# Kernel tuning notes

Hardware: AMD Instinct MI355X
Metric: run time of the kernel (lower is better)

## Reference

```python
import jax, jax.numpy as jnp
import numpy as np

M = 6           # Anderson memory slots (init default)
THRESHOLD = 30  # max forward iterations (forward default)
LAM = 1e-4      # Tikhonov regularization lambda
BETA = 1.0      # learn_beta=False -> beta=1.0 every step


def setup_inputs() -> dict:
    key = jax.random.key(0)
    k1, k2, k3 = jax.random.split(key, 3)
    bsz, d = 2048, 2048
    x0 = jax.random.normal(k1, (bsz, d), jnp.float32)
    # f(x) = tanh(x @ W + b): a contraction-ish layer standing in for the user-supplied f
    W = jax.random.normal(k2, (d, d), jnp.float32) * 0.02
    b = jax.random.normal(k3, (d,), jnp.float32)
    return {"x0": x0, "W": W, "b": b}


def reference(x0, W, b):
    def f(x):
        return jnp.tanh(x @ W + b)

    bsz, d = x0.shape
    m, threshold, lam, beta = M, THRESHOLD, LAM, BETA

    # Eval-mode circular buffers of size m (self.training == False branch)
    X = jnp.zeros((bsz, m, d), x0.dtype).at[:, 0].set(x0)
    F = jnp.zeros((bsz, m, d), x0.dtype).at[:, 0].set(f(x0))
    # torch: F = F.detach(); X = X.detach() (initial entries carry no grad)
    X = jax.lax.stop_gradient(X)
    F = jax.lax.stop_gradient(F)

    # x0 is random nonzero -> (x0 == 0).all() is False -> k_start = 1
    abs_trace, rel_trace = [], []
    eye_m = jnp.eye(m, dtype=x0.dtype)
    up = 0
    for k in range(1, threshold):  # fixed-count unrolled loop; n is static per step
        n = min(k, m)
        up = k % m
        G = F[:, :n] - X[:, :n]                                  # [bsz, n, d]
        GGt = jnp.einsum('bnd,bmd->bnm', G, G) + lam * eye_m[:n, :n]
        # Bordered system H: [[0, 1^T], [1, GG^T + lam I]], y = e_0
        H = (jnp.zeros((bsz, n + 1, n + 1), x0.dtype)
             .at[:, 0, 1:].set(1.0)
             .at[:, 1:, 0].set(1.0)
             .at[:, 1:, 1:].set(GGt))
        y = jnp.zeros((bsz, n + 1, 1), x0.dtype).at[:, 0, 0].set(1.0)
        alpha = jnp.linalg.solve(H, y)[:, 1:, 0]                 # [bsz, n]
        xnew = (beta * jnp.einsum('bn,bnd->bd', alpha, F[:, :n])
                + (1.0 - beta) * jnp.einsum('bn,bnd->bd', alpha, X[:, :n]))
        fnew = f(xnew)
        X = X.at[:, up].set(xnew)
        F = F.at[:, up].set(fnew)
        gx = fnew - xnew
        abs_diff = jnp.linalg.norm(gx)
        rel_diff = abs_diff / (1e-5 + jnp.linalg.norm(fnew))
        abs_trace.append(abs_diff)
        rel_trace.append(rel_diff)

    result = X[:, up]  # 'result' in the torch dict
    rel = jnp.stack(rel_trace).reshape(1, -1)
    absd = jnp.stack(abs_trace).reshape(1, -1)
    return result, X, rel, absd
```

## Files before the change

kernel.cpp:

```cpp
#include <hip/hip_runtime.h>
#include <math.h>

#define BSZ 2048
#define DIM 2048
#define MS 6
#define NIT 29
#define LAMREG 1e-4f
#define XROWS (MS*DIM)

typedef __bf16 bf16x8 __attribute__((ext_vector_type(8)));
typedef __bf16 bf16x4 __attribute__((ext_vector_type(4)));
typedef float  f32x4  __attribute__((ext_vector_type(4)));

__device__ __forceinline__ void async16(const void* g, void* l) {
    __builtin_amdgcn_global_load_lds((const __attribute__((address_space(1))) void*)g,
                                     (__attribute__((address_space(3))) void*)l, 16, 0, 0);
}

__device__ __forceinline__ int swz(int r, int q) {
    return r * 32 + ((q ^ ((r >> 1) & 3)) << 3);
}

__global__ __launch_bounds__(256) void init_kernel(const float* __restrict__ x0,
                                                   float* __restrict__ Xout,
                                                   __bf16* __restrict__ Ahi,
                                                   __bf16* __restrict__ Alo,
                                                   float* __restrict__ norms) {
    int idx = blockIdx.x * 256 + threadIdx.x;
    if (idx < 2 * NIT) norms[idx] = 0.0f;
    for (int i = idx; i < BSZ * DIM; i += gridDim.x * 256) {
        int b = i >> 11;
        int j = i & (DIM - 1);
        float v = x0[i];
        Xout[(size_t)b * XROWS + j] = v;
        __bf16 h = (__bf16)v;
        Ahi[i] = h;
        Alo[i] = (__bf16)(v - (float)h);
    }
}

__global__ __launch_bounds__(256) void wt_split_kernel(const float* __restrict__ W,
                                                       __bf16* __restrict__ WThi,
                                                       __bf16* __restrict__ WTlo) {
    __shared__ float tile[32][33];
    const int tx = threadIdx.x & 31;
    const int ty = threadIdx.x >> 5;
    const int n0 = blockIdx.x * 32;
    const int k0 = blockIdx.y * 32;
#pragma unroll
    for (int i = 0; i < 32; i += 8)
        tile[ty + i][tx] = W[(size_t)(k0 + ty + i) * DIM + n0 + tx];
    __syncthreads();
#pragma unroll
    for (int i = 0; i < 32; i += 8) {
        float v = tile[tx][ty + i];
        __bf16 h = (__bf16)v;
        size_t o = (size_t)(n0 + ty + i) * DIM + k0 + tx;
        WThi[o] = h;
        WTlo[o] = (__bf16)(v - (float)h);
    }
}

__global__ __launch_bounds__(256, 2) void gemm_mfma_kernel(
    const __bf16* __restrict__ Ahi, const __bf16* __restrict__ Alo,
    const __bf16* __restrict__ WThi, const __bf16* __restrict__ WTlo,
    const float* __restrict__ bias,
    const float* __restrict__ Xbase, float* __restrict__ Fbase,
    float* __restrict__ Gbase, int up,
    float* __restrict__ normAcc, int doNorm)
{
    __shared__ __align__(16) __bf16 Ah[2][128 * 32];
    __shared__ __align__(16) __bf16 Al[2][128 * 32];
    __shared__ __align__(16) __bf16 Bh[2][64 * 32];
    __shared__ __align__(16) __bf16 Bl[2][64 * 32];
    __shared__ float rs[8];

    const int id = blockIdx.x;
    const int xcd = id & 7;
    const int slot = id >> 3;
    const int by = ((xcd & 1) << 3) | (slot & 7);
    const int bx = ((xcd >> 1) << 3) | (slot >> 3);
    const int m0 = by * 128;
    const int n0 = bx * 64;

    const int tid = threadIdx.x;
    const int l = tid & 63;
    const int w = tid >> 6;
    const int wm = (w & 1) * 64;
    const int wn = (w >> 1) * 32;
    const int rl = l & 15;
    const int quad = l >> 4;

    const int srow = w * 16 + (l >> 2);
    const int gchunk = (l & 3) ^ ((l >> 3) & 3);
    const int scol = gchunk << 3;
    const size_t aoff = (size_t)(m0 + srow) * DIM + scol;
    const size_t boff = (size_t)(n0 + srow) * DIM + scol;
    const int lo = w * 512;

    f32x4 acc[4][2];
#pragma unroll
    for (int t = 0; t < 4; t++)
#pragma unroll
        for (int u = 0; u < 2; u++) acc[t][u] = (f32x4){0.f, 0.f, 0.f, 0.f};

    auto stage = [&](int kb, int s) {
        async16(Ahi + aoff + kb, &Ah[s][lo]);
        async16(Ahi + aoff + (size_t)64 * DIM + kb, &Ah[s][lo + 2048]);
        async16(Alo + aoff + kb, &Al[s][lo]);
        async16(Alo + aoff + (size_t)64 * DIM + kb, &Al[s][lo + 2048]);
        async16(WThi + boff + kb, &Bh[s][lo]);
        async16(WTlo + boff + kb, &Bl[s][lo]);
    };
    auto compute = [&](int s) {
        bf16x8 ah[4], al[4];
#pragma unroll
        for (int t = 0; t < 4; t++) {
            const int r = wm + t * 16 + rl;
            ah[t] = *(const bf16x8*)&Ah[s][swz(r, quad)];
            al[t] = *(const bf16x8*)&Al[s][swz(r, quad)];
        }
#pragma unroll
        for (int u = 0; u < 2; u++) {
            const int c = wn + u * 16 + rl;
            bf16x8 bh = *(const bf16x8*)&Bh[s][swz(c, quad)];
            bf16x8 bl = *(const bf16x8*)&Bl[s][swz(c, quad)];
#pragma unroll
            for (int t = 0; t < 4; t++) {
                acc[t][u] = __builtin_amdgcn_mfma_f32_16x16x32_bf16(ah[t], bh, acc[t][u], 0, 0, 0);
                acc[t][u] = __builtin_amdgcn_mfma_f32_16x16x32_bf16(al[t], bh, acc[t][u], 0, 0, 0);
                acc[t][u] = __builtin_amdgcn_mfma_f32_16x16x32_bf16(ah[t], bl, acc[t][u], 0, 0, 0);
            }
        }
    };

    stage(0, 0);
    for (int k0 = 0; k0 < DIM; k0 += 64) {
        __syncthreads();
        stage(k0 + 32, 1);
        compute(0);
        __syncthreads();
        if (k0 + 64 < DIM) stage(k0 + 64, 0);
        compute(1);
    }

    int cols[2]; float bv[2];
#pragma unroll
    for (int u = 0; u < 2; u++) {
        cols[u] = n0 + wn + u * 16 + rl;
        bv[u] = bias[cols[u]];
    }
    float s1 = 0.0f, s2 = 0.0f;
#pragma unroll
    for (int t = 0; t < 4; t++) {
#pragma unroll
        for (int r = 0; r < 4; r++) {
            const int row = m0 + wm + t * 16 + quad * 4 + r;
            const size_t base = (size_t)row * XROWS + (size_t)up * DIM;
#pragma unroll
            for (int u = 0; u < 2; u++) {
                float v = tanhf(acc[t][u][r] + bv[u]);
                float xv = Xbase[base + cols[u]];
                float g = v - xv;
                Fbase[base + cols[u]] = v;
                if (Gbase) Gbase[base + cols[u]] = g;
                if (doNorm) { s1 = fmaf(g, g, s1); s2 = fmaf(v, v, s2); }
            }
        }
    }
    if (doNorm) {
#pragma unroll
        for (int off = 32; off > 0; off >>= 1) {
            s1 += __shfl_down(s1, off);
            s2 += __shfl_down(s2, off);
        }
        if (l == 0) { rs[w * 2] = s1; rs[w * 2 + 1] = s2; }
        __syncthreads();
        if (tid == 0) {
            atomicAdd(&normAcc[0], rs[0] + rs[2] + rs[4] + rs[6]);
            atomicAdd(&normAcc[1], rs[1] + rs[3] + rs[5] + rs[7]);
        }
    }
}

__global__ __launch_bounds__(256) void dots_solve_kernel(
    const float* __restrict__ F, const float* __restrict__ X,
    const float* __restrict__ G, float* __restrict__ GGt,
    float* __restrict__ alpha, int up, int nact)
{
    const int b = blockIdx.x;
    const int tid = threadIdx.x;
    const size_t rb = (size_t)b * XROWS;
    float acc[MS];
#pragma unroll
    for (int p = 0; p < MS; p++) acc[p] = 0.0f;

    if (G) {
        const f32x4* Gb = (const f32x4*)(G + rb);
        for (int pos = tid; pos < DIM / 4; pos += 256) {
            f32x4 gu = Gb[up * (DIM / 4) + pos];
#pragma unroll
            for (int j = 0; j < MS; j++) {
                if (j < nact) {
                    f32x4 gj = (j == up) ? gu : Gb[j * (DIM / 4) + pos];
                    acc[j] = fmaf(gu.x, gj.x, acc[j]);
                    acc[j] = fmaf(gu.y, gj.y, acc[j]);
                    acc[j] = fmaf(gu.z, gj.z, acc[j]);
                    acc[j] = fmaf(gu.w, gj.w, acc[j]);
                }
            }
        }
    } else {
        const f32x4* Fb = (const f32x4*)(F + rb);
        const f32x4* Xb = (const f32x4*)(X + rb);
        for (int pos = tid; pos < DIM / 4; pos += 256) {
            f32x4 fu = Fb[up * (DIM / 4) + pos];
            f32x4 xu = Xb[up * (DIM / 4) + pos];
            f32x4 gu = fu - xu;
#pragma unroll
            for (int j = 0; j < MS; j++) {
                if (j < nact) {
                    f32x4 gj;
                    if (j == up) gj = gu;
                    else {
                        f32x4 fj = Fb[j * (DIM / 4) + pos];
                        f32x4 xj = Xb[j * (DIM / 4) + pos];
                        gj = fj - xj;
                    }
                    acc[j] = fmaf(gu.x, gj.x, acc[j]);
                    acc[j] = fmaf(gu.y, gj.y, acc[j]);
                    acc[j] = fmaf(gu.z, gj.z, acc[j]);
                    acc[j] = fmaf(gu.w, gj.w, acc[j]);
                }
            }
        }
    }

#pragma unroll
    for (int p = 0; p < MS; p++) {
        float v = acc[p];
#pragma unroll
        for (int off = 32; off > 0; off >>= 1) v += __shfl_down(v, off);
        acc[p] = v;
    }
    __shared__ float red[4][MS];
    __shared__ float Hs[7][8];
    __shared__ float sols[7];
    const int lane = tid & 63, wave = tid >> 6;
    if (lane == 0) {
#pragma unroll
        for (int p = 0; p < MS; p++) red[wave][p] = acc[p];
    }
    __syncthreads();
    if (tid == 0) {
        float d[MS];
#pragma unroll
        for (int j = 0; j < MS; j++)
            d[j] = red[0][j] + red[1][j] + red[2][j] + red[3][j];
        float* gg = GGt + (size_t)b * 36;
        for (int j = 0; j < nact; j++) {
            gg[up * 6 + j] = d[j];
            gg[j * 6 + up] = d[j];
        }
        const int np = nact + 1;
        for (int i = 0; i < np; i++) {
            for (int j = 0; j < np; j++) {
                float v;
                if (i == 0 && j == 0) v = 0.0f;
                else if (i == 0 || j == 0) v = 1.0f;
                else {
                    v = gg[(i - 1) * 6 + (j - 1)];
                    if (i == j) v += LAMREG;
                }
                Hs[i][j] = v;
            }
            Hs[i][7] = (i == 0) ? 1.0f : 0.0f;
        }
        for (int c = 0; c < np; c++) {
            int piv = c;
            float mx = fabsf(Hs[c][c]);
            for (int r = c + 1; r < np; r++) {
                float a = fabsf(Hs[r][c]);
                if (a > mx) { mx = a; piv = r; }
            }
            if (piv != c) {
                for (int cc = c; cc <= 7; cc++) {
                    float t = Hs[c][cc]; Hs[c][cc] = Hs[piv][cc]; Hs[piv][cc] = t;
                }
            }
            float inv = 1.0f / Hs[c][c];
            for (int r = c + 1; r < np; r++) {
                float f = Hs[r][c] * inv;
                for (int cc = c; cc <= 7; cc++) Hs[r][cc] -= f * Hs[c][cc];
            }
        }
        for (int c = np - 1; c >= 0; c--) {
            float s = Hs[c][7];
            for (int cc = c + 1; cc < np; cc++) s -= Hs[c][cc] * sols[cc];
            sols[c] = s / Hs[c][c];
        }
        for (int i = 0; i < nact; i++) alpha[(size_t)b * MS + i] = sols[i + 1];
    }
}

__global__ __launch_bounds__(256) void xnew_kernel(
    const float* __restrict__ F, const float* __restrict__ alpha,
    float* __restrict__ Xout, __bf16* __restrict__ Ahi, __bf16* __restrict__ Alo,
    float* __restrict__ resultOrNull, int n, int up)
{
    const int idx = blockIdx.x * 256 + threadIdx.x;
    const int b = idx >> 9;
    const int j4 = idx & 511;
    const float* al = alpha + (size_t)b * MS;
    const f32x4* fb = (const f32x4*)(F + (size_t)b * XROWS);
    f32x4 s = (f32x4){0.f, 0.f, 0.f, 0.f};
    for (int i = 0; i < n; i++) {
        f32x4 fv = fb[i * (DIM / 4) + j4];
        float a = al[i];
        s.x = fmaf(a, fv.x, s.x);
        s.y = fmaf(a, fv.y, s.y);
        s.z = fmaf(a, fv.z, s.z);
        s.w = fmaf(a, fv.w, s.w);
    }
    *(f32x4*)(Xout + (size_t)b * XROWS + (size_t)up * DIM + (size_t)j4 * 4) = s;
    if (resultOrNull) ((f32x4*)resultOrNull)[idx] = s;
    bf16x4 hh, ll;
#pragma unroll
    for (int c = 0; c < 4; c++) {
        float v = s[c];
        __bf16 h = (__bf16)v;
        hh[c] = h;
        ll[c] = (__bf16)(v - (float)h);
    }
    *(bf16x4*)&Ahi[(size_t)idx * 4] = hh;
    *(bf16x4*)&Alo[(size_t)idx * 4] = ll;
}

__global__ void finalize_kernel(const float* __restrict__ norms,
                                float* __restrict__ rel, float* __restrict__ absd)
{
    int t = threadIdx.x;
    if (t < NIT) {
        float a = sqrtf(norms[2 * t]);
        float fn = sqrtf(norms[2 * t + 1]);
        absd[t] = a;
        rel[t] = a / (1e-5f + fn);
    }
}

extern "C" void kernel_launch(void* const* d_in, const int* in_sizes, int n_in,
                              void* d_out, int out_size, void* d_ws, size_t ws_size,
                              hipStream_t stream) {
    const float* x0   = (const float*)d_in[0];
    const float* W    = (const float*)d_in[1];
    const float* bias = (const float*)d_in[2];

    float* out    = (float*)d_out;
    float* result = out;
    float* Xout   = out + (size_t)BSZ * DIM;
    float* rel    = Xout + (size_t)BSZ * MS * DIM;
    float* absd   = rel + NIT;

    char* ws = (char*)d_ws;
    float* F     = (float*)ws;
    float* alpha = F + (size_t)BSZ * MS * DIM;
    float* norms = alpha + (size_t)BSZ * MS;
    float* GGt   = norms + 64;
    char* p = (char*)(GGt + (size_t)BSZ * 36);
    size_t off = ((size_t)(p - ws) + 255) & ~(size_t)255;
    __bf16* Ahi  = (__bf16*)(ws + off);  off += (size_t)BSZ * DIM * 2;
    __bf16* Alo  = (__bf16*)(ws + off);  off += (size_t)BSZ * DIM * 2;
    __bf16* WThi = (__bf16*)(ws + off);  off += (size_t)DIM * DIM * 2;
    __bf16* WTlo = (__bf16*)(ws + off);  off += (size_t)DIM * DIM * 2;
    float* G = nullptr;
    if (ws_size >= off + (size_t)BSZ * MS * DIM * 4 + 256) {
        off = (off + 255) & ~(size_t)255;
        G = (float*)(ws + off);
    }

    wt_split_kernel<<<dim3(64, 64), 256, 0, stream>>>(W, WThi, WTlo);
    init_kernel<<<2048, 256, 0, stream>>>(x0, Xout, Ahi, Alo, norms);
    gemm_mfma_kernel<<<512, 256, 0, stream>>>(Ahi, Alo, WThi, WTlo, bias,
                                              Xout, F, G, 0, nullptr, 0);
    dots_solve_kernel<<<BSZ, 256, 0, stream>>>(F, Xout, G, GGt, alpha, 0, 1);
    for (int k = 1; k <= NIT; k++) {
        int n = (k < MS) ? k : MS;
        int up = k % MS;
        int nact = (k + 1 < MS) ? (k + 1) : MS;
        xnew_kernel<<<BSZ * DIM / 1024, 256, 0, stream>>>(F, alpha, Xout, Ahi, Alo,
                                                          (k == NIT) ? result : nullptr,
                                                          n, up);
        gemm_mfma_kernel<<<512, 256, 0, stream>>>(Ahi, Alo, WThi, WTlo, bias,
                                                  Xout, F, G, up,
                                                  norms + 2 * (k - 1), 1);
        if (k < NIT)
            dots_solve_kernel<<<BSZ, 256, 0, stream>>>(F, Xout, G, GGt, alpha, up, nact);
    }
    finalize_kernel<<<1, 64, 0, stream>>>(norms, rel, absd);
}
```

Before: 4.469 ms.

## Split-K GEMM with 128x128 tiles and fuse epilogue, dots, solve, xnew per row

The GEMM now uses 128x128 tiles with a 2-way split over K and writes raw fp32 partials to a scratch buffer. A new per-row mega kernel sums the partials, adds the bias and applies tanh, writes F and G, computes the Gram dot products and norms, solves the small bordered system, and forms the next x with its bf16 hi/lo split. This replaces three kernels per iteration with two. It removes the separate xnew pass and repeated F reads, and spreads the norm atomics over 8 slots. In exchange it adds a round trip of two full fp32 partial matrices through memory, and the serial solve now sits inside a kernel that also streams row data.

```diff
diff --git a/kernel.cpp b/kernel.cpp
--- a/kernel.cpp
+++ b/kernel.cpp
@@ -7,6 +7,7 @@
 #define NIT 29
 #define LAMREG 1e-4f
 #define XROWS (MS*DIM)
+#define N2 ((size_t)BSZ*DIM)
 
 typedef __bf16 bf16x8 __attribute__((ext_vector_type(8)));
 typedef __bf16 bf16x4 __attribute__((ext_vector_type(4)));
@@ -27,7 +28,7 @@
                                                    __bf16* __restrict__ Alo,
                                                    float* __restrict__ norms) {
     int idx = blockIdx.x * 256 + threadIdx.x;
-    if (idx < 2 * NIT) norms[idx] = 0.0f;
+    if (idx < 16 * NIT) norms[idx] = 0.0f;
     for (int i = idx; i < BSZ * DIM; i += gridDim.x * 256) {
         int b = i >> 11;
         int j = i & (DIM - 1);
@@ -64,45 +65,44 @@
 __global__ __launch_bounds__(256, 2) void gemm_mfma_kernel(
     const __bf16* __restrict__ Ahi, const __bf16* __restrict__ Alo,
     const __bf16* __restrict__ WThi, const __bf16* __restrict__ WTlo,
-    const float* __restrict__ bias,
-    const float* __restrict__ Xbase, float* __restrict__ Fbase,
-    float* __restrict__ Gbase, int up,
-    float* __restrict__ normAcc, int doNorm)
+    float* __restrict__ P)
 {
     __shared__ __align__(16) __bf16 Ah[2][128 * 32];
     __shared__ __align__(16) __bf16 Al[2][128 * 32];
-    __shared__ __align__(16) __bf16 Bh[2][64 * 32];
-    __shared__ __align__(16) __bf16 Bl[2][64 * 32];
-    __shared__ float rs[8];
+    __shared__ __align__(16) __bf16 Bh[2][128 * 32];
+    __shared__ __align__(16) __bf16 Bl[2][128 * 32];
 
     const int id = blockIdx.x;
     const int xcd = id & 7;
-    const int slot = id >> 3;
-    const int by = ((xcd & 1) << 3) | (slot & 7);
-    const int bx = ((xcd >> 1) << 3) | (slot >> 3);
+    const int rest = id >> 3;
+    const int ks = rest >> 5;
+    const int slot = rest & 31;
+    const int by = ((xcd & 3) << 2) | (slot & 3);
+    const int bx = ((xcd >> 2) << 3) | (slot >> 2);
     const int m0 = by * 128;
-    const int n0 = bx * 64;
+    const int n0 = bx * 128;
+    const int kbase = ks << 10;
 
     const int tid = threadIdx.x;
     const int l = tid & 63;
     const int w = tid >> 6;
     const int wm = (w & 1) * 64;
-    const int wn = (w >> 1) * 32;
+    const int wn = (w >> 1) * 64;
     const int rl = l & 15;
     const int quad = l >> 4;
 
     const int srow = w * 16 + (l >> 2);
     const int gchunk = (l & 3) ^ ((l >> 3) & 3);
     const int scol = gchunk << 3;
-    const size_t aoff = (size_t)(m0 + srow) * DIM + scol;
-    const size_t boff = (size_t)(n0 + srow) * DIM + scol;
+    const size_t aoff = (size_t)(m0 + srow) * DIM + kbase + scol;
+    const size_t boff = (size_t)(n0 + srow) * DIM + kbase + scol;
     const int lo = w * 512;
 
-    f32x4 acc[4][2];
+    f32x4 acc[4][4];
 #pragma unroll
     for (int t = 0; t < 4; t++)
 #pragma unroll
-        for (int u = 0; u < 2; u++) acc[t][u] = (f32x4){0.f, 0.f, 0.f, 0.f};
+        for (int u = 0; u < 4; u++) acc[t][u] = (f32x4){0.f, 0.f, 0.f, 0.f};
 
     auto stage = [&](int kb, int s) {
         async16(Ahi + aoff + kb, &Ah[s][lo]);
@@ -110,7 +110,9 @@
         async16(Alo + aoff + kb, &Al[s][lo]);
         async16(Alo + aoff + (size_t)64 * DIM + kb, &Al[s][lo + 2048]);
         async16(WThi + boff + kb, &Bh[s][lo]);
+        async16(WThi + boff + (size_t)64 * DIM + kb, &Bh[s][lo + 2048]);
         async16(WTlo + boff + kb, &Bl[s][lo]);
+        async16(WTlo + boff + (size_t)64 * DIM + kb, &Bl[s][lo + 2048]);
     };
     auto compute = [&](int s) {
         bf16x8 ah[4], al[4];
@@ -121,7 +123,7 @@
             al[t] = *(const bf16x8*)&Al[s][swz(r, quad)];
         }
 #pragma unroll
-        for (int u = 0; u < 2; u++) {
+        for (int u = 0; u < 4; u++) {
             const int c = wn + u * 16 + rl;
             bf16x8 bh = *(const bf16x8*)&Bh[s][swz(c, quad)];
             bf16x8 bl = *(const bf16x8*)&Bl[s][swz(c, quad)];
@@ -135,205 +137,217 @@
     };
 
     stage(0, 0);
-    for (int k0 = 0; k0 < DIM; k0 += 64) {
+    for (int k0 = 0; k0 < 1024; k0 += 64) {
         __syncthreads();
         stage(k0 + 32, 1);
         compute(0);
         __syncthreads();
-        if (k0 + 64 < DIM) stage(k0 + 64, 0);
+        if (k0 + 64 < 1024) stage(k0 + 64, 0);
         compute(1);
     }
 
-    int cols[2]; float bv[2];
-#pragma unroll
-    for (int u = 0; u < 2; u++) {
-        cols[u] = n0 + wn + u * 16 + rl;
-        bv[u] = bias[cols[u]];
-    }
-    float s1 = 0.0f, s2 = 0.0f;
+    float* Pk = P + (size_t)ks * N2;
 #pragma unroll
     for (int t = 0; t < 4; t++) {
 #pragma unroll
         for (int r = 0; r < 4; r++) {
             const int row = m0 + wm + t * 16 + quad * 4 + r;
-            const size_t base = (size_t)row * XROWS + (size_t)up * DIM;
-#pragma unroll
-            for (int u = 0; u < 2; u++) {
-                float v = tanhf(acc[t][u][r] + bv[u]);
-                float xv = Xbase[base + cols[u]];
-                float g = v - xv;
-                Fbase[base + cols[u]] = v;
-                if (Gbase) Gbase[base + cols[u]] = g;
-                if (doNorm) { s1 = fmaf(g, g, s1); s2 = fmaf(v, v, s2); }
-            }
-        }
-    }
-    if (doNorm) {
-#pragma unroll
-        for (int off = 32; off > 0; off >>= 1) {
-            s1 += __shfl_down(s1, off);
-            s2 += __shfl_down(s2, off);
-        }
-        if (l == 0) { rs[w * 2] = s1; rs[w * 2 + 1] = s2; }
-        __syncthreads();
-        if (tid == 0) {
-            atomicAdd(&normAcc[0], rs[0] + rs[2] + rs[4] + rs[6]);
-            atomicAdd(&normAcc[1], rs[1] + rs[3] + rs[5] + rs[7]);
-        }
-    }
-}
-
-__global__ __launch_bounds__(256) void dots_solve_kernel(
-    const float* __restrict__ F, const float* __restrict__ X,
-    const float* __restrict__ G, float* __restrict__ GGt,
-    float* __restrict__ alpha, int up, int nact)
+            float* pr = Pk + (size_t)row * DIM + n0 + wn;
+#pragma unroll
+            for (int u = 0; u < 4; u++) pr[u * 16 + rl] = acc[t][u][r];
+        }
+    }
+}
+
+__global__ __launch_bounds__(256) void mega_kernel(
+    const float* __restrict__ P, const float* __restrict__ bias,
+    float* __restrict__ Fb, float* __restrict__ Xb, float* __restrict__ Gb,
+    float* __restrict__ GGt,
+    __bf16* __restrict__ Ahi, __bf16* __restrict__ Alo,
+    float* __restrict__ resultOrNull, float* __restrict__ normAcc,
+    int up, int nact, int nxt)
 {
     const int b = blockIdx.x;
     const int tid = threadIdx.x;
     const size_t rb = (size_t)b * XROWS;
-    float acc[MS];
-#pragma unroll
-    for (int p = 0; p < MS; p++) acc[p] = 0.0f;
-
-    if (G) {
-        const f32x4* Gb = (const f32x4*)(G + rb);
-        for (int pos = tid; pos < DIM / 4; pos += 256) {
-            f32x4 gu = Gb[up * (DIM / 4) + pos];
-#pragma unroll
-            for (int j = 0; j < MS; j++) {
-                if (j < nact) {
-                    f32x4 gj = (j == up) ? gu : Gb[j * (DIM / 4) + pos];
-                    acc[j] = fmaf(gu.x, gj.x, acc[j]);
-                    acc[j] = fmaf(gu.y, gj.y, acc[j]);
-                    acc[j] = fmaf(gu.z, gj.z, acc[j]);
-                    acc[j] = fmaf(gu.w, gj.w, acc[j]);
-                }
-            }
-        }
-    } else {
-        const f32x4* Fb = (const f32x4*)(F + rb);
-        const f32x4* Xb = (const f32x4*)(X + rb);
-        for (int pos = tid; pos < DIM / 4; pos += 256) {
-            f32x4 fu = Fb[up * (DIM / 4) + pos];
-            f32x4 xu = Xb[up * (DIM / 4) + pos];
-            f32x4 gu = fu - xu;
-#pragma unroll
-            for (int j = 0; j < MS; j++) {
-                if (j < nact) {
-                    f32x4 gj;
-                    if (j == up) gj = gu;
-                    else {
-                        f32x4 fj = Fb[j * (DIM / 4) + pos];
-                        f32x4 xj = Xb[j * (DIM / 4) + pos];
-                        gj = fj - xj;
+    const size_t prow = (size_t)b * DIM;
+
+    const f32x4* P0 = (const f32x4*)(P + prow);
+    const f32x4* P1 = (const f32x4*)(P + N2 + prow);
+    const f32x4* Bi = (const f32x4*)bias;
+    const f32x4* Xu = (const f32x4*)(Xb + rb + (size_t)up * DIM);
+    f32x4* Fu = (f32x4*)(Fb + rb + (size_t)up * DIM);
+    f32x4* Gu = Gb ? (f32x4*)(Gb + rb + (size_t)up * DIM) : nullptr;
+
+    f32x4 fv[2], gv[2];
+    float s1 = 0.f, s2 = 0.f;
+#pragma unroll
+    for (int i = 0; i < 2; i++) {
+        const int p4 = tid + 256 * i;
+        f32x4 z = P0[p4] + P1[p4] + Bi[p4];
+        f32x4 t;
+        t.x = tanhf(z.x); t.y = tanhf(z.y); t.z = tanhf(z.z); t.w = tanhf(z.w);
+        f32x4 xv = Xu[p4];
+        f32x4 g = t - xv;
+        fv[i] = t; gv[i] = g;
+        Fu[p4] = t;
+        if (Gu) Gu[p4] = g;
+        s1 += g.x * g.x + g.y * g.y + g.z * g.z + g.w * g.w;
+        s2 += t.x * t.x + t.y * t.y + t.z * t.z + t.w * t.w;
+    }
+
+    float acc[8];
+#pragma unroll
+    for (int p = 0; p < MS; p++) acc[p] = 0.f;
+    acc[6] = s1; acc[7] = s2;
+
+    if (nact > 0) {
+#pragma unroll
+        for (int j = 0; j < MS; j++) {
+            if (j < nact) {
+                if (j == up) { acc[j] = s1; continue; }
+                float a = 0.f;
+                if (Gb) {
+                    const f32x4* Gj = (const f32x4*)(Gb + rb + (size_t)j * DIM);
+#pragma unroll
+                    for (int i = 0; i < 2; i++) {
+                        const int p4 = tid + 256 * i;
+                        f32x4 gj = Gj[p4];
+                        a += gv[i].x * gj.x + gv[i].y * gj.y + gv[i].z * gj.z + gv[i].w * gj.w;
                     }
-                    acc[j] = fmaf(gu.x, gj.x, acc[j]);
-                    acc[j] = fmaf(gu.y, gj.y, acc[j]);
-                    acc[j] = fmaf(gu.z, gj.z, acc[j]);
-                    acc[j] = fmaf(gu.w, gj.w, acc[j]);
-                }
-            }
-        }
-    }
-
-#pragma unroll
-    for (int p = 0; p < MS; p++) {
+                } else {
+                    const f32x4* Fj = (const f32x4*)(Fb + rb + (size_t)j * DIM);
+                    const f32x4* Xj = (const f32x4*)(Xb + rb + (size_t)j * DIM);
+#pragma unroll
+                    for (int i = 0; i < 2; i++) {
+                        const int p4 = tid + 256 * i;
+                        f32x4 gj = Fj[p4] - Xj[p4];
+                        a += gv[i].x * gj.x + gv[i].y * gj.y + gv[i].z * gj.z + gv[i].w * gj.w;
+                    }
+                }
+                acc[j] = a;
+            }
+        }
+    }
+
+#pragma unroll
+    for (int p = 0; p < 8; p++) {
         float v = acc[p];
 #pragma unroll
         for (int off = 32; off > 0; off >>= 1) v += __shfl_down(v, off);
         acc[p] = v;
     }
-    __shared__ float red[4][MS];
+    __shared__ float red[4][8];
     __shared__ float Hs[7][8];
-    __shared__ float sols[7];
+    __shared__ float alf[7];
     const int lane = tid & 63, wave = tid >> 6;
     if (lane == 0) {
 #pragma unroll
-        for (int p = 0; p < MS; p++) red[wave][p] = acc[p];
+        for (int p = 0; p < 8; p++) red[wave][p] = acc[p];
     }
     __syncthreads();
+
     if (tid == 0) {
-        float d[MS];
-#pragma unroll
-        for (int j = 0; j < MS; j++)
-            d[j] = red[0][j] + red[1][j] + red[2][j] + red[3][j];
-        float* gg = GGt + (size_t)b * 36;
-        for (int j = 0; j < nact; j++) {
-            gg[up * 6 + j] = d[j];
-            gg[j * 6 + up] = d[j];
-        }
-        const int np = nact + 1;
-        for (int i = 0; i < np; i++) {
-            for (int j = 0; j < np; j++) {
-                float v;
-                if (i == 0 && j == 0) v = 0.0f;
-                else if (i == 0 || j == 0) v = 1.0f;
-                else {
-                    v = gg[(i - 1) * 6 + (j - 1)];
-                    if (i == j) v += LAMREG;
-                }
-                Hs[i][j] = v;
-            }
-            Hs[i][7] = (i == 0) ? 1.0f : 0.0f;
-        }
-        for (int c = 0; c < np; c++) {
-            int piv = c;
-            float mx = fabsf(Hs[c][c]);
-            for (int r = c + 1; r < np; r++) {
-                float a = fabsf(Hs[r][c]);
-                if (a > mx) { mx = a; piv = r; }
-            }
-            if (piv != c) {
-                for (int cc = c; cc <= 7; cc++) {
-                    float t = Hs[c][cc]; Hs[c][cc] = Hs[piv][cc]; Hs[piv][cc] = t;
-                }
-            }
-            float inv = 1.0f / Hs[c][c];
-            for (int r = c + 1; r < np; r++) {
-                float f = Hs[r][c] * inv;
-                for (int cc = c; cc <= 7; cc++) Hs[r][cc] -= f * Hs[c][cc];
-            }
-        }
-        for (int c = np - 1; c >= 0; c--) {
-            float s = Hs[c][7];
-            for (int cc = c + 1; cc < np; cc++) s -= Hs[c][cc] * sols[cc];
-            sols[c] = s / Hs[c][c];
-        }
-        for (int i = 0; i < nact; i++) alpha[(size_t)b * MS + i] = sols[i + 1];
-    }
-}
-
-__global__ __launch_bounds__(256) void xnew_kernel(
-    const float* __restrict__ F, const float* __restrict__ alpha,
-    float* __restrict__ Xout, __bf16* __restrict__ Ahi, __bf16* __restrict__ Alo,
-    float* __restrict__ resultOrNull, int n, int up)
-{
-    const int idx = blockIdx.x * 256 + threadIdx.x;
-    const int b = idx >> 9;
-    const int j4 = idx & 511;
-    const float* al = alpha + (size_t)b * MS;
-    const f32x4* fb = (const f32x4*)(F + (size_t)b * XROWS);
-    f32x4 s = (f32x4){0.f, 0.f, 0.f, 0.f};
-    for (int i = 0; i < n; i++) {
-        f32x4 fv = fb[i * (DIM / 4) + j4];
-        float a = al[i];
-        s.x = fmaf(a, fv.x, s.x);
-        s.y = fmaf(a, fv.y, s.y);
-        s.z = fmaf(a, fv.z, s.z);
-        s.w = fmaf(a, fv.w, s.w);
-    }
-    *(f32x4*)(Xout + (size_t)b * XROWS + (size_t)up * DIM + (size_t)j4 * 4) = s;
-    if (resultOrNull) ((f32x4*)resultOrNull)[idx] = s;
-    bf16x4 hh, ll;
-#pragma unroll
-    for (int c = 0; c < 4; c++) {
-        float v = s[c];
-        __bf16 h = (__bf16)v;
-        hh[c] = h;
-        ll[c] = (__bf16)(v - (float)h);
-    }
-    *(bf16x4*)&Ahi[(size_t)idx * 4] = hh;
-    *(bf16x4*)&Alo[(size_t)idx * 4] = ll;
+        float d[8];
+#pragma unroll
+        for (int p = 0; p < 8; p++)
+            d[p] = red[0][p] + red[1][p] + red[2][p] + red[3][p];
+        if (normAcc) {
+            atomicAdd(&normAcc[b & 7], d[6]);
+            atomicAdd(&normAcc[8 + (b & 7)], d[7]);
+        }
+        if (nact > 0) {
+            float* gg = GGt + (size_t)b * 36;
+            for (int j = 0; j < nact; j++) {
+                gg[up * 6 + j] = d[j];
+                gg[j * 6 + up] = d[j];
+            }
+            const int np = nact + 1;
+            for (int i = 0; i < np; i++) {
+                for (int j = 0; j < np; j++) {
+                    float v;
+                    if (i == 0 && j == 0) v = 0.0f;
+                    else if (i == 0 || j == 0) v = 1.0f;
+                    else {
+                        v = gg[(i - 1) * 6 + (j - 1)];
+                        if (i == j) v += LAMREG;
+                    }
+                    Hs[i][j] = v;
+                }
+                Hs[i][7] = (i == 0) ? 1.0f : 0.0f;
+            }
+            for (int c = 0; c < np; c++) {
+                int piv = c;
+                float mx = fabsf(Hs[c][c]);
+                for (int r = c + 1; r < np; r++) {
+                    float a = fabsf(Hs[r][c]);
+                    if (a > mx) { mx = a; piv = r; }
+                }
+                if (piv != c) {
+                    for (int cc = c; cc <= 7; cc++) {
+                        float t = Hs[c][cc]; Hs[c][cc] = Hs[piv][cc]; Hs[piv][cc] = t;
+                    }
+                }
+                float inv = 1.0f / Hs[c][c];
+                for (int r = c + 1; r < np; r++) {
+                    float f = Hs[r][c] * inv;
+                    for (int cc = c; cc <= 7; cc++) Hs[r][cc] -= f * Hs[c][cc];
+                }
+            }
+            float sol[7];
+            for (int c = np - 1; c >= 0; c--) {
+                float s = Hs[c][7];
+                for (int cc = c + 1; cc < np; cc++) s -= Hs[c][cc] * sol[cc];
+                sol[c] = s / Hs[c][c];
+            }
+            for (int i = 0; i < nact; i++) alf[i] = sol[i + 1];
+        }
+    }
+    __syncthreads();
+
+    if (nxt >= 0) {
+        f32x4 s[2] = {(f32x4){0.f,0.f,0.f,0.f}, (f32x4){0.f,0.f,0.f,0.f}};
+        for (int i2 = 0; i2 < nact; i2++) {
+            const float a = alf[i2];
+            if (i2 == up) {
+#pragma unroll
+                for (int i = 0; i < 2; i++) {
+                    s[i].x = fmaf(a, fv[i].x, s[i].x);
+                    s[i].y = fmaf(a, fv[i].y, s[i].y);
+                    s[i].z = fmaf(a, fv[i].z, s[i].z);
+                    s[i].w = fmaf(a, fv[i].w, s[i].w);
+                }
+            } else {
+                const f32x4* Fi = (const f32x4*)(Fb + rb + (size_t)i2 * DIM);
+#pragma unroll
+                for (int i = 0; i < 2; i++) {
+                    const int p4 = tid + 256 * i;
+                    f32x4 fj = Fi[p4];
+                    s[i].x = fmaf(a, fj.x, s[i].x);
+                    s[i].y = fmaf(a, fj.y, s[i].y);
+                    s[i].z = fmaf(a, fj.z, s[i].z);
+                    s[i].w = fmaf(a, fj.w, s[i].w);
+                }
+            }
+        }
+        f32x4* Xn = (f32x4*)(Xb + rb + (size_t)nxt * DIM);
+#pragma unroll
+        for (int i = 0; i < 2; i++) {
+            const int p4 = tid + 256 * i;
+            Xn[p4] = s[i];
+            if (resultOrNull) ((f32x4*)(resultOrNull + prow))[p4] = s[i];
+            bf16x4 hh, ll;
+#pragma unroll
+            for (int c = 0; c < 4; c++) {
+                float v = s[i][c];
+                __bf16 h = (__bf16)v;
+                hh[c] = h;
+                ll[c] = (__bf16)(v - (float)h);
+            }
+            *(bf16x4*)&Ahi[prow + (size_t)p4 * 4] = hh;
+            *(bf16x4*)&Alo[prow + (size_t)p4 * 4] = ll;
+        }
+    }
 }
 
 __global__ void finalize_kernel(const float* __restrict__ norms,
@@ -341,10 +355,14 @@
 {
     int t = threadIdx.x;
     if (t < NIT) {
-        float a = sqrtf(norms[2 * t]);
-        float fn = sqrtf(norms[2 * t + 1]);
+        float a2 = 0.f, f2 = 0.f;
+        for (int i = 0; i < 8; i++) {
+            a2 += norms[t * 16 + i];
+            f2 += norms[t * 16 + 8 + i];
+        }
+        float a = sqrtf(a2);
         absd[t] = a;
-        rel[t] = a / (1e-5f + fn);
+        rel[t] = a / (1e-5f + sqrtf(f2));
     }
 }
 
@@ -363,10 +381,10 @@
 
     char* ws = (char*)d_ws;
     float* F     = (float*)ws;
-    float* alpha = F + (size_t)BSZ * MS * DIM;
-    float* norms = alpha + (size_t)BSZ * MS;
-    float* GGt   = norms + 64;
-    char* p = (char*)(GGt + (size_t)BSZ * 36);
+    float* norms = F + (size_t)BSZ * MS * DIM;
+    float* GGt   = norms + 512;
+    float* P     = GGt + (size_t)BSZ * 36;
+    char* p = (char*)(P + 2 * N2);
     size_t off = ((size_t)(p - ws) + 255) & ~(size_t)255;
     __bf16* Ahi  = (__bf16*)(ws + off);  off += (size_t)BSZ * DIM * 2;
     __bf16* Alo  = (__bf16*)(ws + off);  off += (size_t)BSZ * DIM * 2;
@@ -380,21 +398,16 @@
 
     wt_split_kernel<<<dim3(64, 64), 256, 0, stream>>>(W, WThi, WTlo);
     init_kernel<<<2048, 256, 0, stream>>>(x0, Xout, Ahi, Alo, norms);
-    gemm_mfma_kernel<<<512, 256, 0, stream>>>(Ahi, Alo, WThi, WTlo, bias,
-                                              Xout, F, G, 0, nullptr, 0);
-    dots_solve_kernel<<<BSZ, 256, 0, stream>>>(F, Xout, G, GGt, alpha, 0, 1);
-    for (int k = 1; k <= NIT; k++) {
-        int n = (k < MS) ? k : MS;
-        int up = k % MS;
-        int nact = (k + 1 < MS) ? (k + 1) : MS;
-        xnew_kernel<<<BSZ * DIM / 1024, 256, 0, stream>>>(F, alpha, Xout, Ahi, Alo,
-                                                          (k == NIT) ? result : nullptr,
-                                                          n, up);
-        gemm_mfma_kernel<<<512, 256, 0, stream>>>(Ahi, Alo, WThi, WTlo, bias,
-                                                  Xout, F, G, up,
-                                                  norms + 2 * (k - 1), 1);
-        if (k < NIT)
-            dots_solve_kernel<<<BSZ, 256, 0, stream>>>(F, Xout, G, GGt, alpha, up, nact);
+
+    for (int j = 0; j <= NIT; j++) {
+        gemm_mfma_kernel<<<512, 256, 0, stream>>>(Ahi, Alo, WThi, WTlo, P);
+        int up   = j % MS;
+        int nact = (j < NIT) ? ((j + 1 < MS) ? (j + 1) : MS) : 0;
+        int nxt  = (j < NIT) ? ((j + 1) % MS) : -1;
+        mega_kernel<<<BSZ, 256, 0, stream>>>(P, bias, F, Xout, G, GGt, Ahi, Alo,
+                                             (j == NIT - 1) ? result : nullptr,
+                                             (j >= 1) ? (norms + 16 * (j - 1)) : nullptr,
+                                             up, nact, nxt);
     }
     finalize_kernel<<<1, 64, 0, stream>>>(norms, rel, absd);
 }
```

New measurement: 4.587 ms. 2.6% more time.
